# Performance work log

Measured on AMD Instinct MI355X. Metric: run time of the kernel, lower is better.

The kernel has to match this reference:

```python
import jax, jax.numpy as jnp
import numpy as np

N_NODES = 100000
N_EDGES = 1600000
F_IN = 128
HID = 64
N_CLS = 40


def _sage_conv(x, src, dst, Wl, bl, Wr, num_nodes):
    # PyG SAGEConv (aggr='mean', root_weight=True, normalize=False):
    # out = lin_l(mean_{j in N(i)} x_j) + lin_r(x_i)
    msg = x[src]                                              # [E, F] gather
    agg = jax.ops.segment_sum(msg, dst, num_segments=num_nodes)
    deg = jax.ops.segment_sum(jnp.ones_like(dst, dtype=x.dtype), dst,
                              num_segments=num_nodes)
    mean = agg / jnp.maximum(deg, 1.0)[:, None]               # [N, F]
    return mean @ Wl.T + bl + x @ Wr.T


def setup_inputs() -> dict:
    key = jax.random.key(0)
    ks = jax.random.split(key, 16)

    def lin(k, out_d, in_d):
        bound = 1.0 / np.sqrt(in_d)
        return jax.random.uniform(k, (out_d, in_d), jnp.float32, -bound, bound)

    x = jax.random.normal(ks[0], (N_NODES, F_IN), jnp.float32)
    edge_index = jax.random.randint(ks[1], (2, N_EDGES), 0, N_NODES, jnp.int64)

    return {
        "x": x,
        "edge_index": edge_index,
        "W1l": lin(ks[2], HID, F_IN), "b1": jnp.zeros((HID,), jnp.float32),
        "W1r": lin(ks[3], HID, F_IN),
        "W2l": lin(ks[4], HID, HID), "b2": jnp.zeros((HID,), jnp.float32),
        "W2r": lin(ks[5], HID, HID),
        "W3l": lin(ks[6], HID, HID), "b3": jnp.zeros((HID,), jnp.float32),
        "W3r": lin(ks[7], HID, HID),
        "Wout": lin(ks[8], N_CLS, HID),
        "bout": jnp.zeros((N_CLS,), jnp.float32),
    }


def reference(x, edge_index, W1l, b1, W1r, W2l, b2, W2r, W3l, b3, W3r, Wout, bout):
    src, dst = edge_index[0], edge_index[1]
    n = x.shape[0]
    h = _sage_conv(x, src, dst, W1l, b1, W1r, n)
    h = jax.nn.elu(h)
    h = _sage_conv(h, src, dst, W2l, b2, W2r, n)
    h = jax.nn.elu(h)
    h = _sage_conv(h, src, dst, W3l, b3, W3r, n)
    return h @ Wout.T + bout
```

## Files before the change

kernel.cpp:

```cpp
#include <hip/hip_runtime.h>


static inline size_t ws_align(size_t x) { return (x + 511) & ~size_t(511); }

#define MAXBC  104
#define CAPL   96
#define EB_CAP 24576

using frag_ab = __attribute__((ext_vector_type(8))) short;
using f32x4   = __attribute__((ext_vector_type(4))) float;
using us4     = __attribute__((ext_vector_type(4))) unsigned short;

__device__ inline short f2bf(float f) {
    unsigned u = __builtin_bit_cast(unsigned, f);
    u += 0x7fff + ((u >> 16) & 1);
    return (short)(u >> 16);
}
__device__ inline float b2f(unsigned short h) {
    unsigned u = ((unsigned)h) << 16;
    return __builtin_bit_cast(float, u);
}


__global__ void zero_kernel(int* __restrict__ p, int n) {
    int i = blockIdx.x * blockDim.x + threadIdx.x;
    if (i < n) p[i] = 0;
}

__global__ void prep_all(const float* __restrict__ W1l, const float* __restrict__ W1r,
                         const float* __restrict__ W2l, const float* __restrict__ W2r,
                         const float* __restrict__ W3l, const float* __restrict__ W3r,
                         unsigned short* __restrict__ fw) {
    const int idx = blockIdx.x * 256 + threadIdx.x;
    if (idx >= 32768) return;
    const float* W;
    unsigned short* out;
    int F, rel;
    if (idx < 8192)       { W = W1l; out = fw;        F = 128; rel = idx; }
    else if (idx < 16384) { W = W1r; out = fw + 8192; F = 128; rel = idx - 8192; }
    else {
        const int q = (idx - 16384) >> 12;
        rel = (idx - 16384) & 4095;
        F = 64;
        W = (q == 0) ? W2l : (q == 1) ? W2r : (q == 2) ? W3l : W3r;
        out = fw + 16384 + q * 4096;
    }
    const int k = rel % F;
    const int col = rel / F;
    out[(k >> 3) * 512 + col * 8 + (k & 7)] = (unsigned short)f2bf(W[rel]);
}


__global__ void pass1_bin(const int* __restrict__ src, const int* __restrict__ dst,
                          int* __restrict__ bcur, unsigned* __restrict__ ebuf,
                          int nE, int nN, int nbc) {
    __shared__ unsigned lbuf[MAXBC][CAPL];
    __shared__ int bcnt[MAXBC];
    __shared__ int gbase[MAXBC];
    const int t = threadIdx.x;
    const int e0 = blockIdx.x * 4096;
    for (int i = t; i < MAXBC; i += 256) bcnt[i] = 0;
    __syncthreads();
#pragma unroll
    for (int q = 0; q < 16; ++q) {
        const int e = e0 + q * 256 + t;
        if (e < nE) {
            const unsigned d = (unsigned)dst[e];
            const unsigned s = (unsigned)src[e];
            if (d < (unsigned)nN && s < (unsigned)nN) {
                const int cb = (int)(d >> 10);
                const unsigned v = ((d & 1023u) << 17) | s;
                const int pos = atomicAdd(&bcnt[cb], 1);
                if (pos < CAPL) {
                    lbuf[cb][pos] = v;
                } else {
                    const int gp = atomicAdd(&bcur[cb], 1);
                    if (gp < EB_CAP) ebuf[(size_t)cb * EB_CAP + gp] = v;
                }
            }
        }
    }
    __syncthreads();
    for (int b = t; b < nbc; b += 256) {
        const int cnt = min(bcnt[b], CAPL);
        bcnt[b] = cnt;
        gbase[b] = (cnt > 0) ? atomicAdd(&bcur[b], cnt) : 0;
    }
    __syncthreads();
    const int wid = t >> 6, lane = t & 63;
    for (int b = wid; b < nbc; b += 4) {
        const int cnt = bcnt[b];
        const int gb = gbase[b];
        for (int i = lane; i < cnt; i += 64) {
            const int gp = gb + i;
            if (gp < EB_CAP) ebuf[(size_t)b * EB_CAP + gp] = lbuf[b][i];
        }
    }
}

__global__ void scan_buckets(const int* __restrict__ bcur, int* __restrict__ bbase, int nbc) {
    __shared__ int sdata[256];
    const int t = threadIdx.x;
    const int v = (t < nbc) ? min(bcur[t], EB_CAP) : 0;
    sdata[t] = v;
    __syncthreads();
    for (int off = 1; off < 256; off <<= 1) {
        int add = (t >= off) ? sdata[t - off] : 0;
        __syncthreads();
        sdata[t] += add;
        __syncthreads();
    }
    if (t < nbc) bbase[t] = sdata[t] - v;
}

__global__ void pass2_build(const unsigned* __restrict__ ebuf,
                            const int* __restrict__ bcur, const int* __restrict__ bbase,
                            int* __restrict__ rowptr, int* __restrict__ csr,
                            int nN, int nbc) {
    __shared__ int lcnt[1024];
    __shared__ int lcur[1024];
    __shared__ int sdata[256];
    const int b = blockIdx.x;
    const int node0 = b << 10;
    const int nloc = min(1024, nN - node0);
    if (nloc <= 0) return;
    const int cnt  = min(bcur[b], EB_CAP);
    const int base = bbase[b];
    const int t = threadIdx.x;
    const unsigned* eb = ebuf + (size_t)b * EB_CAP;

    for (int i = t; i < 1024; i += 256) lcnt[i] = 0;
    __syncthreads();
    for (int i = t; i < cnt; i += 256) atomicAdd(&lcnt[eb[i] >> 17], 1);
    __syncthreads();
    int v[4];
    int tsum = 0;
#pragma unroll
    for (int q = 0; q < 4; ++q) { v[q] = lcnt[t * 4 + q]; tsum += v[q]; }
    sdata[t] = tsum;
    __syncthreads();
    for (int off = 1; off < 256; off <<= 1) {
        int add = (t >= off) ? sdata[t - off] : 0;
        __syncthreads();
        sdata[t] += add;
        __syncthreads();
    }
    int run = sdata[t] - tsum;
#pragma unroll
    for (int q = 0; q < 4; ++q) {
        const int l = t * 4 + q;
        lcur[l] = run;
        if (l < nloc) rowptr[node0 + l] = base + run;
        run += v[q];
    }
    if (b == nbc - 1 && t == 0) rowptr[nN] = base + cnt;
    __syncthreads();
    for (int i = t; i < cnt; i += 256) {
        const unsigned ev = eb[i];
        const int pos = atomicAdd(&lcur[ev >> 17], 1);
        csr[base + pos] = (int)((ev & 0x1FFFFu) << 7);
    }
}

template<int F, bool AF32>
__global__ void proj2_mfma(const void* __restrict__ Aptr,
                           const unsigned short* __restrict__ fwl,
                           const unsigned short* __restrict__ fwr,
                           const float* __restrict__ bias,
                           unsigned short* __restrict__ xl,
                           unsigned short* __restrict__ xr,
                           int nN) {
    const int t    = threadIdx.x;
    const int wave = t >> 6;
    const int lane = t & 63;
    const int lg   = lane >> 4;
    const int lr   = lane & 15;
    const int row0 = blockIdx.x * 64 + wave * 16;

    const float*          Af = (const float*)Aptr;
    const unsigned short* Ab = (const unsigned short*)Aptr;

    f32x4 accl[4] = {};
    f32x4 accr[4] = {};

#pragma unroll
    for (int ks = 0; ks < F / 32; ++ks) {
        const int k0 = ks * 32 + lg * 8;
        frag_ab afr;
        {
            int row = row0 + lr;
            if (row >= nN) row = nN - 1;
            if constexpr (AF32) {
                const float4 f0 = *reinterpret_cast<const float4*>(Af + (size_t)row * F + k0);
                const float4 f1 = *reinterpret_cast<const float4*>(Af + (size_t)row * F + k0 + 4);
                afr[0] = f2bf(f0.x); afr[1] = f2bf(f0.y); afr[2] = f2bf(f0.z); afr[3] = f2bf(f0.w);
                afr[4] = f2bf(f1.x); afr[5] = f2bf(f1.y); afr[6] = f2bf(f1.z); afr[7] = f2bf(f1.w);
            } else {
                afr = *reinterpret_cast<const frag_ab*>(Ab + (size_t)row * F + k0);
            }
        }
        const int ob = (ks * 4 + lg) * 512;
#pragma unroll
        for (int nf = 0; nf < 4; ++nf) {
            const int col = nf * 16 + lr;
            const frag_ab bl = *reinterpret_cast<const frag_ab*>(fwl + ob + col * 8);
            const frag_ab br = *reinterpret_cast<const frag_ab*>(fwr + ob + col * 8);
            accl[nf] = __builtin_amdgcn_mfma_f32_16x16x32_bf16(afr, bl, accl[nf], 0, 0, 0);
            accr[nf] = __builtin_amdgcn_mfma_f32_16x16x32_bf16(afr, br, accr[nf], 0, 0, 0);
        }
    }

#pragma unroll
    for (int nf = 0; nf < 4; ++nf) {
        const int col = nf * 16 + lr;
        const float bv = bias[col];
#pragma unroll
        for (int j = 0; j < 4; ++j) {
            const int row = row0 + lg * 4 + j;
            if (row < nN) {
                xl[(size_t)row * 64 + col] = (unsigned short)f2bf(accl[nf][j]);
                xr[(size_t)row * 64 + col] = (unsigned short)f2bf(accr[nf][j] + bv);
            }
        }
    }
}

template<bool DOELU>
__global__ void gather_kernel(const unsigned short* __restrict__ xl,
                              const unsigned short* __restrict__ xr,
                              const int* __restrict__ rowptr, const int* __restrict__ csr,
                              unsigned short* __restrict__ outp, int nN, int nE) {
    const int node = blockIdx.x * (blockDim.x >> 6) + (threadIdx.x >> 6);
    if (node >= nN) return;
    const int lane = threadIdx.x & 63;
    int b = rowptr[node];
    int e = rowptr[node + 1];
    b = max(0, min(b, nE));
    e = max(b, min(e, nE));
    b = __builtin_amdgcn_readfirstlane(b);
    e = __builtin_amdgcn_readfirstlane(e);
    const float d = (float)(e - b);
    const char* xlb = (const char*)xl + (lane << 1);

    float acc = 0.f;
    int i = b;
    for (; i + 16 <= e; i += 16) {
        unsigned short v[16];
#pragma unroll
        for (int j = 0; j < 16; ++j) {
            const unsigned s = (unsigned)csr[i + j];
            v[j] = *(const unsigned short*)(xlb + s);
        }
#pragma unroll
        for (int j = 0; j < 16; ++j) acc += b2f(v[j]);
    }
    if (i < e) {
        const int lim = e - i;
        unsigned short v[16];
#pragma unroll
        for (int j = 0; j < 16; ++j) {
            const unsigned s = (unsigned)csr[i + min(j, lim - 1)];
            v[j] = *(const unsigned short*)(xlb + s);
        }
#pragma unroll
        for (int j = 0; j < 16; ++j) acc += (j < lim) ? b2f(v[j]) : 0.f;
    }

    float vout = acc / fmaxf(d, 1.0f) + b2f(xr[(size_t)node * 64 + lane]);
    if (DOELU) vout = vout > 0.f ? vout : expm1f(vout);
    outp[(size_t)node * 64 + lane] = (unsigned short)f2bf(vout);
}

template<int F, int NOUT>
__global__ void head_kernel(const unsigned short* __restrict__ A,
                            const float* __restrict__ W,
                            const float* __restrict__ bias,
                            float* __restrict__ out, int nN) {
    constexpr int NCH = F / 32;
    __shared__ float As[64][36];
    __shared__ float Bs[32][64];

    const int t = threadIdx.x;
    const int block0 = blockIdx.x * 64;
    const int tm = (t >> 4) << 2;
    const int tn = (t & 15) << 2;

    float acc[4][4] = {};

    for (int ch = 0; ch < NCH; ++ch) {
        const int kg0 = ch * 32;
        {
            const int kk = (t & 7) * 4;
#pragma unroll
            for (int r = 0; r < 2; ++r) {
                const int n = (t >> 3) + r * 32;
                const int node = block0 + n;
                float4 v = make_float4(0.f, 0.f, 0.f, 0.f);
                if (node < nN) {
                    const us4 u = *reinterpret_cast<const us4*>(A + (size_t)node * F + kg0 + kk);
                    v.x = b2f(u[0]); v.y = b2f(u[1]); v.z = b2f(u[2]); v.w = b2f(u[3]);
                }
                *reinterpret_cast<float4*>(&As[n][kk]) = v;
            }
        }
        {
            const int j = t & 63;
#pragma unroll
            for (int p = 0; p < 8; ++p) {
                const int kk = (t >> 6) + p * 4;
                Bs[kk][j] = (j < NOUT) ? W[(size_t)j * F + kg0 + kk] : 0.0f;
            }
        }
        __syncthreads();
#pragma unroll
        for (int kk = 0; kk < 32; ++kk) {
            const float a0 = As[tm + 0][kk];
            const float a1 = As[tm + 1][kk];
            const float a2 = As[tm + 2][kk];
            const float a3 = As[tm + 3][kk];
            const float4 bv = *reinterpret_cast<const float4*>(&Bs[kk][tn]);
            acc[0][0] += a0 * bv.x; acc[0][1] += a0 * bv.y; acc[0][2] += a0 * bv.z; acc[0][3] += a0 * bv.w;
            acc[1][0] += a1 * bv.x; acc[1][1] += a1 * bv.y; acc[1][2] += a1 * bv.z; acc[1][3] += a1 * bv.w;
            acc[2][0] += a2 * bv.x; acc[2][1] += a2 * bv.y; acc[2][2] += a2 * bv.z; acc[2][3] += a2 * bv.w;
            acc[3][0] += a3 * bv.x; acc[3][1] += a3 * bv.y; acc[3][2] += a3 * bv.z; acc[3][3] += a3 * bv.w;
        }
        __syncthreads();
    }

#pragma unroll
    for (int i = 0; i < 4; ++i) {
        const int node = block0 + tm + i;
        if (node >= nN) continue;
#pragma unroll
        for (int j = 0; j < 4; ++j) {
            const int col = tn + j;
            if (col < NOUT)
                out[(size_t)node * NOUT + col] = acc[i][j] + bias[col];
        }
    }
}


extern "C" void kernel_launch(void* const* d_in, const int* in_sizes, int n_in,
                              void* d_out, int out_size, void* d_ws, size_t ws_size,
                              hipStream_t stream) {
    const float* x    = (const float*)d_in[0];
    const int*   ei   = (const int*)d_in[1];
    const float* W1l  = (const float*)d_in[2];
    const float* b1   = (const float*)d_in[3];
    const float* W1r  = (const float*)d_in[4];
    const float* W2l  = (const float*)d_in[5];
    const float* b2   = (const float*)d_in[6];
    const float* W2r  = (const float*)d_in[7];
    const float* W3l  = (const float*)d_in[8];
    const float* b3   = (const float*)d_in[9];
    const float* W3r  = (const float*)d_in[10];
    const float* Wout = (const float*)d_in[11];
    const float* bout = (const float*)d_in[12];

    const int N = in_sizes[0] / 128;
    const int E = in_sizes[1] / 2;
    const int* src  = ei;
    const int* dstA = ei + E;
    const int nbc = (N + 1023) >> 10;

    char* ws = (char*)d_ws;
    size_t o = 0;
    int* bcur    = (int*)(ws + o); o += ws_align((size_t)MAXBC * 4);
    int* bbase   = (int*)(ws + o); o += ws_align((size_t)MAXBC * 4);
    int* rowptr  = (int*)(ws + o); o += ws_align((size_t)(N + 1) * 4);
    int* csr     = (int*)(ws + o); o += ws_align((size_t)E * 4);
    unsigned* ebuf = (unsigned*)(ws + o); o += ws_align((size_t)MAXBC * EB_CAP * 4);
    unsigned short* fw  = (unsigned short*)(ws + o); o += ws_align((size_t)32768 * 2);
    unsigned short* xl  = (unsigned short*)(ws + o); o += ws_align((size_t)N * 64 * 2);
    unsigned short* xr  = (unsigned short*)(ws + o); o += ws_align((size_t)N * 64 * 2);
    unsigned short* hAb = (unsigned short*)(ws + o); o += ws_align((size_t)N * 64 * 2);
    unsigned short* hBb = (unsigned short*)(ws + o); o += ws_align((size_t)N * 64 * 2);
    unsigned short* h3b = (unsigned short*)(ws + o); o += ws_align((size_t)N * 64 * 2);
    float* outp = (float*)d_out;

    const int projGrid = (N + 63) / 64;
    const int gatherGrid = (N + 3) / 4;
    const int headGrid = (N + 63) / 64;

    zero_kernel<<<1, 256, 0, stream>>>(bcur, MAXBC);
    prep_all<<<128, 256, 0, stream>>>(W1l, W1r, W2l, W2r, W3l, W3r, fw);
    pass1_bin<<<(E + 4095) / 4096, 256, 0, stream>>>(src, dstA, bcur, ebuf, E, N, nbc);
    scan_buckets<<<1, 256, 0, stream>>>(bcur, bbase, nbc);
    pass2_build<<<nbc, 256, 0, stream>>>(ebuf, bcur, bbase, rowptr, csr, N, nbc);

    const unsigned short* fw1l = fw;
    const unsigned short* fw1r = fw + 8192;
    const unsigned short* fw2l = fw + 16384;
    const unsigned short* fw2r = fw + 16384 + 4096;
    const unsigned short* fw3l = fw + 16384 + 8192;
    const unsigned short* fw3r = fw + 16384 + 12288;

    proj2_mfma<128, true><<<projGrid, 256, 0, stream>>>(x, fw1l, fw1r, b1, xl, xr, N);
    gather_kernel<true><<<gatherGrid, 256, 0, stream>>>(xl, xr, rowptr, csr, hAb, N, E);

    proj2_mfma<64, false><<<projGrid, 256, 0, stream>>>(hAb, fw2l, fw2r, b2, xl, xr, N);
    gather_kernel<true><<<gatherGrid, 256, 0, stream>>>(xl, xr, rowptr, csr, hBb, N, E);

    proj2_mfma<64, false><<<projGrid, 256, 0, stream>>>(hBb, fw3l, fw3r, b3, xl, xr, N);
    gather_kernel<false><<<gatherGrid, 256, 0, stream>>>(xl, xr, rowptr, csr, h3b, N, E);

    head_kernel<64, 40><<<headGrid, 256, 0, stream>>>(h3b, Wout, bout, outp, N);
}
```

Measured before the change: 274.0 us.

## Merge setup kernels, co-launch edge binning with layer-1 projection, MFMA head

Folds the bucket-counter zeroing into the weight-prep kernel and adds bf16 packing of the output weights. Edge binning and the first-layer projection now run in one launch, with block ranges split between the two independent jobs. The bucket scan moves into pass2_build, where each block recomputes it redundantly. The scalar fp32 head GEMM becomes a bf16 MFMA kernel. The aim is fewer launches and serial gaps, plus overlap of binning with the projection, at the cost of bf16 rounding in the head.

Measured after the change: 240.7 us. -12.1%, faster.

```diff
diff --git a/kernel.cpp b/kernel.cpp
--- a/kernel.cpp
+++ b/kernel.cpp
@@ -9,7 +9,6 @@
 
 using frag_ab = __attribute__((ext_vector_type(8))) short;
 using f32x4   = __attribute__((ext_vector_type(4))) float;
-using us4     = __attribute__((ext_vector_type(4))) unsigned short;
 
 __device__ inline short f2bf(float f) {
     unsigned u = __builtin_bit_cast(unsigned, f);
@@ -21,44 +20,47 @@
     return __builtin_bit_cast(float, u);
 }
 
-
-__global__ void zero_kernel(int* __restrict__ p, int n) {
-    int i = blockIdx.x * blockDim.x + threadIdx.x;
-    if (i < n) p[i] = 0;
-}
-
-__global__ void prep_all(const float* __restrict__ W1l, const float* __restrict__ W1r,
-                         const float* __restrict__ W2l, const float* __restrict__ W2r,
-                         const float* __restrict__ W3l, const float* __restrict__ W3r,
-                         unsigned short* __restrict__ fw) {
+__global__ void setup_kernel(const float* __restrict__ W1l, const float* __restrict__ W1r,
+                             const float* __restrict__ W2l, const float* __restrict__ W2r,
+                             const float* __restrict__ W3l, const float* __restrict__ W3r,
+                             const float* __restrict__ Wout,
+                             unsigned short* __restrict__ fw, int* __restrict__ bcur) {
     const int idx = blockIdx.x * 256 + threadIdx.x;
-    if (idx >= 32768) return;
-    const float* W;
-    unsigned short* out;
-    int F, rel;
-    if (idx < 8192)       { W = W1l; out = fw;        F = 128; rel = idx; }
-    else if (idx < 16384) { W = W1r; out = fw + 8192; F = 128; rel = idx - 8192; }
-    else {
-        const int q = (idx - 16384) >> 12;
-        rel = (idx - 16384) & 4095;
-        F = 64;
-        W = (q == 0) ? W2l : (q == 1) ? W2r : (q == 2) ? W3l : W3r;
-        out = fw + 16384 + q * 4096;
-    }
-    const int k = rel % F;
-    const int col = rel / F;
-    out[(k >> 3) * 512 + col * 8 + (k & 7)] = (unsigned short)f2bf(W[rel]);
-}
-
-
-__global__ void pass1_bin(const int* __restrict__ src, const int* __restrict__ dst,
-                          int* __restrict__ bcur, unsigned* __restrict__ ebuf,
-                          int nE, int nN, int nbc) {
+    if (blockIdx.x == 0 && threadIdx.x < MAXBC) bcur[threadIdx.x] = 0;
+    if (idx >= 36864) return;
+    if (idx < 32768) {
+        const float* W;
+        unsigned short* out;
+        int F, rel;
+        if (idx < 8192)       { W = W1l; out = fw;        F = 128; rel = idx; }
+        else if (idx < 16384) { W = W1r; out = fw + 8192; F = 128; rel = idx - 8192; }
+        else {
+            const int q = (idx - 16384) >> 12;
+            rel = (idx - 16384) & 4095;
+            F = 64;
+            W = (q == 0) ? W2l : (q == 1) ? W2r : (q == 2) ? W3l : W3r;
+            out = fw + 16384 + q * 4096;
+        }
+        const int k = rel % F;
+        const int col = rel / F;
+        out[(k >> 3) * 512 + col * 8 + (k & 7)] = (unsigned short)f2bf(W[rel]);
+    } else {
+        const int rel = idx - 32768;
+        const int col = rel / 64;
+        const int k = rel % 64;
+        const float v = (col < 40) ? Wout[col * 64 + k] : 0.0f;
+        fw[32768 + (k >> 3) * 512 + col * 8 + (k & 7)] = (unsigned short)f2bf(v);
+    }
+}
+
+__device__ __forceinline__ void pass1_body(const int* __restrict__ src, const int* __restrict__ dst,
+                                           int* __restrict__ bcur, unsigned* __restrict__ ebuf,
+                                           int nE, int nN, int nbc, int bid) {
     __shared__ unsigned lbuf[MAXBC][CAPL];
     __shared__ int bcnt[MAXBC];
     __shared__ int gbase[MAXBC];
     const int t = threadIdx.x;
-    const int e0 = blockIdx.x * 4096;
+    const int e0 = bid * 4096;
     for (int i = t; i < MAXBC; i += 256) bcnt[i] = 0;
     __syncthreads();
 #pragma unroll
@@ -98,84 +100,20 @@
     }
 }
 
-__global__ void scan_buckets(const int* __restrict__ bcur, int* __restrict__ bbase, int nbc) {
-    __shared__ int sdata[256];
-    const int t = threadIdx.x;
-    const int v = (t < nbc) ? min(bcur[t], EB_CAP) : 0;
-    sdata[t] = v;
-    __syncthreads();
-    for (int off = 1; off < 256; off <<= 1) {
-        int add = (t >= off) ? sdata[t - off] : 0;
-        __syncthreads();
-        sdata[t] += add;
-        __syncthreads();
-    }
-    if (t < nbc) bbase[t] = sdata[t] - v;
-}
-
-__global__ void pass2_build(const unsigned* __restrict__ ebuf,
-                            const int* __restrict__ bcur, const int* __restrict__ bbase,
-                            int* __restrict__ rowptr, int* __restrict__ csr,
-                            int nN, int nbc) {
-    __shared__ int lcnt[1024];
-    __shared__ int lcur[1024];
-    __shared__ int sdata[256];
-    const int b = blockIdx.x;
-    const int node0 = b << 10;
-    const int nloc = min(1024, nN - node0);
-    if (nloc <= 0) return;
-    const int cnt  = min(bcur[b], EB_CAP);
-    const int base = bbase[b];
-    const int t = threadIdx.x;
-    const unsigned* eb = ebuf + (size_t)b * EB_CAP;
-
-    for (int i = t; i < 1024; i += 256) lcnt[i] = 0;
-    __syncthreads();
-    for (int i = t; i < cnt; i += 256) atomicAdd(&lcnt[eb[i] >> 17], 1);
-    __syncthreads();
-    int v[4];
-    int tsum = 0;
-#pragma unroll
-    for (int q = 0; q < 4; ++q) { v[q] = lcnt[t * 4 + q]; tsum += v[q]; }
-    sdata[t] = tsum;
-    __syncthreads();
-    for (int off = 1; off < 256; off <<= 1) {
-        int add = (t >= off) ? sdata[t - off] : 0;
-        __syncthreads();
-        sdata[t] += add;
-        __syncthreads();
-    }
-    int run = sdata[t] - tsum;
-#pragma unroll
-    for (int q = 0; q < 4; ++q) {
-        const int l = t * 4 + q;
-        lcur[l] = run;
-        if (l < nloc) rowptr[node0 + l] = base + run;
-        run += v[q];
-    }
-    if (b == nbc - 1 && t == 0) rowptr[nN] = base + cnt;
-    __syncthreads();
-    for (int i = t; i < cnt; i += 256) {
-        const unsigned ev = eb[i];
-        const int pos = atomicAdd(&lcur[ev >> 17], 1);
-        csr[base + pos] = (int)((ev & 0x1FFFFu) << 7);
-    }
-}
-
 template<int F, bool AF32>
-__global__ void proj2_mfma(const void* __restrict__ Aptr,
-                           const unsigned short* __restrict__ fwl,
-                           const unsigned short* __restrict__ fwr,
-                           const float* __restrict__ bias,
-                           unsigned short* __restrict__ xl,
-                           unsigned short* __restrict__ xr,
-                           int nN) {
+__device__ __forceinline__ void proj_body(const void* __restrict__ Aptr,
+                                          const unsigned short* __restrict__ fwl,
+                                          const unsigned short* __restrict__ fwr,
+                                          const float* __restrict__ bias,
+                                          unsigned short* __restrict__ xl,
+                                          unsigned short* __restrict__ xr,
+                                          int nN, int bid) {
     const int t    = threadIdx.x;
     const int wave = t >> 6;
     const int lane = t & 63;
     const int lg   = lane >> 4;
     const int lr   = lane & 15;
-    const int row0 = blockIdx.x * 64 + wave * 16;
+    const int row0 = bid * 64 + wave * 16;
 
     const float*          Af = (const float*)Aptr;
     const unsigned short* Ab = (const unsigned short*)Aptr;
@@ -222,6 +160,91 @@
                 xr[(size_t)row * 64 + col] = (unsigned short)f2bf(accr[nf][j] + bv);
             }
         }
+    }
+}
+
+__global__ void fused_p1_proj1(const int* __restrict__ src, const int* __restrict__ dst,
+                               int* __restrict__ bcur, unsigned* __restrict__ ebuf,
+                               int nE, int nN, int nbc, int nbP1,
+                               const float* __restrict__ x,
+                               const unsigned short* __restrict__ fwl,
+                               const unsigned short* __restrict__ fwr,
+                               const float* __restrict__ bias,
+                               unsigned short* __restrict__ xl,
+                               unsigned short* __restrict__ xr) {
+    if ((int)blockIdx.x < nbP1)
+        pass1_body(src, dst, bcur, ebuf, nE, nN, nbc, blockIdx.x);
+    else
+        proj_body<128, true>(x, fwl, fwr, bias, xl, xr, nN, blockIdx.x - nbP1);
+}
+
+template<int F, bool AF32>
+__global__ void proj2_mfma(const void* __restrict__ Aptr,
+                           const unsigned short* __restrict__ fwl,
+                           const unsigned short* __restrict__ fwr,
+                           const float* __restrict__ bias,
+                           unsigned short* __restrict__ xl,
+                           unsigned short* __restrict__ xr,
+                           int nN) {
+    proj_body<F, AF32>(Aptr, fwl, fwr, bias, xl, xr, nN, blockIdx.x);
+}
+
+__global__ void pass2_build(const unsigned* __restrict__ ebuf,
+                            const int* __restrict__ bcur,
+                            int* __restrict__ rowptr, int* __restrict__ csr,
+                            int nN, int nbc) {
+    __shared__ int sc[128];
+    __shared__ int lcnt[1024];
+    __shared__ int lcur[1024];
+    __shared__ int sdata[256];
+    const int b = blockIdx.x;
+    const int node0 = b << 10;
+    const int nloc = min(1024, nN - node0);
+    if (nloc <= 0) return;
+    const int t = threadIdx.x;
+
+    if (t < 128) sc[t] = (t < nbc) ? min(bcur[t], EB_CAP) : 0;
+    __syncthreads();
+    for (int off = 1; off < 128; off <<= 1) {
+        int add = (t < 128 && t >= off) ? sc[t - off] : 0;
+        __syncthreads();
+        if (t < 128) sc[t] += add;
+        __syncthreads();
+    }
+    const int cnt  = min(bcur[b], EB_CAP);
+    const int base = sc[b] - cnt;
+    const unsigned* eb = ebuf + (size_t)b * EB_CAP;
+
+    for (int i = t; i < 1024; i += 256) lcnt[i] = 0;
+    __syncthreads();
+    for (int i = t; i < cnt; i += 256) atomicAdd(&lcnt[eb[i] >> 17], 1);
+    __syncthreads();
+    int v[4];
+    int tsum = 0;
+#pragma unroll
+    for (int q = 0; q < 4; ++q) { v[q] = lcnt[t * 4 + q]; tsum += v[q]; }
+    sdata[t] = tsum;
+    __syncthreads();
+    for (int off = 1; off < 256; off <<= 1) {
+        int add = (t >= off) ? sdata[t - off] : 0;
+        __syncthreads();
+        sdata[t] += add;
+        __syncthreads();
+    }
+    int run = sdata[t] - tsum;
+#pragma unroll
+    for (int q = 0; q < 4; ++q) {
+        const int l = t * 4 + q;
+        lcur[l] = run;
+        if (l < nloc) rowptr[node0 + l] = base + run;
+        run += v[q];
+    }
+    if (b == nbc - 1 && t == 0) rowptr[nN] = base + cnt;
+    __syncthreads();
+    for (int i = t; i < cnt; i += 256) {
+        const unsigned ev = eb[i];
+        const int pos = atomicAdd(&lcur[ev >> 17], 1);
+        csr[base + pos] = (int)((ev & 0x1FFFFu) << 7);
     }
 }
 
@@ -271,71 +294,47 @@
     outp[(size_t)node * 64 + lane] = (unsigned short)f2bf(vout);
 }
 
-template<int F, int NOUT>
-__global__ void head_kernel(const unsigned short* __restrict__ A,
-                            const float* __restrict__ W,
-                            const float* __restrict__ bias,
-                            float* __restrict__ out, int nN) {
-    constexpr int NCH = F / 32;
-    __shared__ float As[64][36];
-    __shared__ float Bs[32][64];
-
-    const int t = threadIdx.x;
-    const int block0 = blockIdx.x * 64;
-    const int tm = (t >> 4) << 2;
-    const int tn = (t & 15) << 2;
-
-    float acc[4][4] = {};
-
-    for (int ch = 0; ch < NCH; ++ch) {
-        const int kg0 = ch * 32;
+__global__ void head_mfma(const unsigned short* __restrict__ A,
+                          const unsigned short* __restrict__ fwo,
+                          const float* __restrict__ bias,
+                          float* __restrict__ out, int nN) {
+    const int t    = threadIdx.x;
+    const int wave = t >> 6;
+    const int lane = t & 63;
+    const int lg   = lane >> 4;
+    const int lr   = lane & 15;
+    const int row0 = blockIdx.x * 64 + wave * 16;
+
+    f32x4 acc[3] = {};
+
+#pragma unroll
+    for (int ks = 0; ks < 2; ++ks) {
+        const int k0 = ks * 32 + lg * 8;
+        frag_ab afr;
         {
-            const int kk = (t & 7) * 4;
-#pragma unroll
-            for (int r = 0; r < 2; ++r) {
-                const int n = (t >> 3) + r * 32;
-                const int node = block0 + n;
-                float4 v = make_float4(0.f, 0.f, 0.f, 0.f);
-                if (node < nN) {
-                    const us4 u = *reinterpret_cast<const us4*>(A + (size_t)node * F + kg0 + kk);
-                    v.x = b2f(u[0]); v.y = b2f(u[1]); v.z = b2f(u[2]); v.w = b2f(u[3]);
-                }
-                *reinterpret_cast<float4*>(&As[n][kk]) = v;
-            }
-        }
-        {
-            const int j = t & 63;
-#pragma unroll
-            for (int p = 0; p < 8; ++p) {
-                const int kk = (t >> 6) + p * 4;
-                Bs[kk][j] = (j < NOUT) ? W[(size_t)j * F + kg0 + kk] : 0.0f;
-            }
-        }
-        __syncthreads();
-#pragma unroll
-        for (int kk = 0; kk < 32; ++kk) {
-            const float a0 = As[tm + 0][kk];
-            const float a1 = As[tm + 1][kk];
-            const float a2 = As[tm + 2][kk];
-            const float a3 = As[tm + 3][kk];
-            const float4 bv = *reinterpret_cast<const float4*>(&Bs[kk][tn]);
-            acc[0][0] += a0 * bv.x; acc[0][1] += a0 * bv.y; acc[0][2] += a0 * bv.z; acc[0][3] += a0 * bv.w;
-            acc[1][0] += a1 * bv.x; acc[1][1] += a1 * bv.y; acc[1][2] += a1 * bv.z; acc[1][3] += a1 * bv.w;
-            acc[2][0] += a2 * bv.x; acc[2][1] += a2 * bv.y; acc[2][2] += a2 * bv.z; acc[2][3] += a2 * bv.w;
-            acc[3][0] += a3 * bv.x; acc[3][1] += a3 * bv.y; acc[3][2] += a3 * bv.z; acc[3][3] += a3 * bv.w;
-        }
-        __syncthreads();
-    }
-
-#pragma unroll
-    for (int i = 0; i < 4; ++i) {
-        const int node = block0 + tm + i;
-        if (node >= nN) continue;
+            int row = row0 + lr;
+            if (row >= nN) row = nN - 1;
+            afr = *reinterpret_cast<const frag_ab*>(A + (size_t)row * 64 + k0);
+        }
+        const int ob = (ks * 4 + lg) * 512;
+#pragma unroll
+        for (int nf = 0; nf < 3; ++nf) {
+            const int col = nf * 16 + lr;
+            const frag_ab bo = *reinterpret_cast<const frag_ab*>(fwo + ob + col * 8);
+            acc[nf] = __builtin_amdgcn_mfma_f32_16x16x32_bf16(afr, bo, acc[nf], 0, 0, 0);
+        }
+    }
+
+#pragma unroll
+    for (int nf = 0; nf < 3; ++nf) {
+        const int col = nf * 16 + lr;
+        if (col >= 40) continue;
+        const float bv = bias[col];
 #pragma unroll
         for (int j = 0; j < 4; ++j) {
-            const int col = tn + j;
-            if (col < NOUT)
-                out[(size_t)node * NOUT + col] = acc[i][j] + bias[col];
+            const int row = row0 + lg * 4 + j;
+            if (row < nN)
+                out[(size_t)row * 40 + col] = acc[nf][j] + bv;
         }
     }
 }
@@ -363,15 +362,15 @@
     const int* src  = ei;
     const int* dstA = ei + E;
     const int nbc = (N + 1023) >> 10;
+    const int nbP1 = (E + 4095) / 4096;
 
     char* ws = (char*)d_ws;
     size_t o = 0;
     int* bcur    = (int*)(ws + o); o += ws_align((size_t)MAXBC * 4);
-    int* bbase   = (int*)(ws + o); o += ws_align((size_t)MAXBC * 4);
     int* rowptr  = (int*)(ws + o); o += ws_align((size_t)(N + 1) * 4);
     int* csr     = (int*)(ws + o); o += ws_align((size_t)E * 4);
     unsigned* ebuf = (unsigned*)(ws + o); o += ws_align((size_t)MAXBC * EB_CAP * 4);
-    unsigned short* fw  = (unsigned short*)(ws + o); o += ws_align((size_t)32768 * 2);
+    unsigned short* fw  = (unsigned short*)(ws + o); o += ws_align((size_t)36864 * 2);
     unsigned short* xl  = (unsigned short*)(ws + o); o += ws_align((size_t)N * 64 * 2);
     unsigned short* xr  = (unsigned short*)(ws + o); o += ws_align((size_t)N * 64 * 2);
     unsigned short* hAb = (unsigned short*)(ws + o); o += ws_align((size_t)N * 64 * 2);
@@ -381,13 +380,6 @@
 
     const int projGrid = (N + 63) / 64;
     const int gatherGrid = (N + 3) / 4;
-    const int headGrid = (N + 63) / 64;
-
-    zero_kernel<<<1, 256, 0, stream>>>(bcur, MAXBC);
-    prep_all<<<128, 256, 0, stream>>>(W1l, W1r, W2l, W2r, W3l, W3r, fw);
-    pass1_bin<<<(E + 4095) / 4096, 256, 0, stream>>>(src, dstA, bcur, ebuf, E, N, nbc);
-    scan_buckets<<<1, 256, 0, stream>>>(bcur, bbase, nbc);
-    pass2_build<<<nbc, 256, 0, stream>>>(ebuf, bcur, bbase, rowptr, csr, N, nbc);
 
     const unsigned short* fw1l = fw;
     const unsigned short* fw1r = fw + 8192;
@@ -395,8 +387,16 @@
     const unsigned short* fw2r = fw + 16384 + 4096;
     const unsigned short* fw3l = fw + 16384 + 8192;
     const unsigned short* fw3r = fw + 16384 + 12288;
-
-    proj2_mfma<128, true><<<projGrid, 256, 0, stream>>>(x, fw1l, fw1r, b1, xl, xr, N);
+    const unsigned short* fwo  = fw + 32768;
+
+    setup_kernel<<<144, 256, 0, stream>>>(W1l, W1r, W2l, W2r, W3l, W3r, Wout, fw, bcur);
+
+    fused_p1_proj1<<<nbP1 + projGrid, 256, 0, stream>>>(
+        src, dstA, bcur, ebuf, E, N, nbc, nbP1,
+        x, fw1l, fw1r, b1, xl, xr);
+
+    pass2_build<<<nbc, 256, 0, stream>>>(ebuf, bcur, rowptr, csr, N, nbc);
+
     gather_kernel<true><<<gatherGrid, 256, 0, stream>>>(xl, xr, rowptr, csr, hAb, N, E);
 
     proj2_mfma<64, false><<<projGrid, 256, 0, stream>>>(hAb, fw2l, fw2r, b2, xl, xr, N);
@@ -405,5 +405,5 @@
     proj2_mfma<64, false><<<projGrid, 256, 0, stream>>>(hBb, fw3l, fw3r, b3, xl, xr, N);
     gather_kernel<false><<<gatherGrid, 256, 0, stream>>>(xl, xr, rowptr, csr, h3b, N, E);
 
-    head_kernel<64, 40><<<headGrid, 256, 0, stream>>>(h3b, Wout, bout, outp, N);
-}
+    head_mfma<<<projGrid, 256, 0, stream>>>(h3b, fwo, bout, outp, N);
+}
```
